# Kernel tuning notes

Measured on AMD Instinct MI355X. Metric: run time of the kernel, lower is better.

## Reference

```python
import jax, jax.numpy as jnp
import numpy as np

B, T, C, H = 4, 2048, 1024, 16
D = C // H  # head dim 64


def setup_inputs() -> dict:
    key = jax.random.key(0)
    ks = jax.random.split(key, 5)
    s = 1.0 / np.sqrt(C)
    return {
        "x": jax.random.normal(ks[0], (B, T, C), jnp.float32),
        "Wq": jax.random.normal(ks[1], (C, C), jnp.float32) * s,
        "bq": jnp.zeros((C,), jnp.float32),
        "Wk": jax.random.normal(ks[2], (C, C), jnp.float32) * s,
        "bk": jnp.zeros((C,), jnp.float32),
        "Wv": jax.random.normal(ks[3], (C, C), jnp.float32) * s,
        "bv": jnp.zeros((C,), jnp.float32),
        "Wp": jax.random.normal(ks[4], (C, C), jnp.float32) * s,
        "bp": jnp.zeros((C,), jnp.float32),
    }


def reference(x, Wq, bq, Wk, bk, Wv, bv, Wp, bp):
    # project and split heads: [B,T,C] -> [B,H,T,D]
    def heads(w, b):
        return (x @ w.T + b).reshape(B, T, H, D).transpose(0, 2, 1, 3)

    q = heads(Wq, bq)
    k = heads(Wk, bk)
    v = heads(Wv, bv)

    att = jnp.einsum("bhqd,bhkd->bhqk", q, k) * (1.0 / np.sqrt(D))
    causal = jnp.tril(jnp.ones((T, T), bool))  # [T,T]
    att = jnp.where(causal[None, None], att, -jnp.inf)
    att = jax.nn.softmax(att, axis=-1)
    # dropout prob is 0.0 -> identity
    y = jnp.einsum("bhqk,bhkd->bhqd", att, v)
    y = y.transpose(0, 2, 1, 3).reshape(B, T, C)
    return y @ Wp.T + bp
```

## Files before the change

### kernel.cpp

```cpp
#include <hip/hip_runtime.h>
#include <hip/hip_bf16.h>

#define BB 4
#define TT 2048
#define CC 1024
#define HH 16
#define DD 64
#define PSTR 72

typedef unsigned short u16;
typedef __attribute__((ext_vector_type(8))) short bf16x8;
typedef __attribute__((ext_vector_type(4))) float f32x4;
typedef __attribute__((ext_vector_type(16))) float f32x16;

__device__ __forceinline__ float bf2f(u16 v) {
    union { unsigned u; float f; } c; c.u = ((unsigned)v) << 16; return c.f;
}
__device__ __forceinline__ u16 f2bf(float f) {
    union { float f; unsigned u; } c; c.f = f;
    unsigned u = c.u + 0x7fffu + ((c.u >> 16) & 1u);
    return (u16)(u >> 16);
}
__device__ __forceinline__ float fast_exp2(float x) {
    float r;
    asm volatile("v_exp_f32 %0, %1\n\ts_nop 1" : "=v"(r) : "v"(x));
    return r;
}
__device__ __forceinline__ unsigned pack_bf16(unsigned b0, unsigned b1) {
    unsigned d;
    asm("v_perm_b32 %0, %1, %2, %3" : "=v"(d) : "v"(b1), "v"(b0), "v"(0x07060302u));
    return d;
}
__device__ __forceinline__ uint2 pack4(float v0, float v1, float v2, float v3) {
    uint2 pk;
    pk.x = pack_bf16(__float_as_uint(v0) + 0x8000u, __float_as_uint(v1) + 0x8000u);
    pk.y = pack_bf16(__float_as_uint(v2) + 0x8000u, __float_as_uint(v3) + 0x8000u);
    return pk;
}
__device__ __forceinline__ void gload16(const u16* g, u16* l) {
    __builtin_amdgcn_global_load_lds(
        (const __attribute__((address_space(1))) void*)g,
        (__attribute__((address_space(3))) void*)l, 16, 0, 0);
}

__device__ __forceinline__ int detect_bf16(const u16* __restrict__ xprobe, int* sh) {
    const int t = threadIdx.x;
    u16 hh = xprobe[2 * t];
    int e = (hh >> 7) & 0xFF;
    unsigned long long m = __ballot(e >= 118 && e <= 132);
    if ((t & 63) == 0) sh[t >> 6] = __popcll(m);
    __syncthreads();
    return (sh[0] + sh[1] + sh[2] + sh[3]) >= 128;
}

struct CastArgs {
    const void* src[9];
    u16* dst[9];
    int blk_start[10];
    int n[9];
};
__global__ __launch_bounds__(256) void cast_all(CastArgs a, const u16* __restrict__ xprobe) {
    __shared__ int sh[4];
    const int isbf = detect_bf16(xprobe, sh);
    int b = blockIdx.x;
    int s = 0;
    while (s < 8 && b >= a.blk_start[s + 1]) s++;
    int i0 = (b - a.blk_start[s]) * 2048 + threadIdx.x * 8;
    if (i0 + 8 > a.n[s]) return;
    if (isbf) {
        *(uint4*)&a.dst[s][i0] = *(const uint4*)&((const u16*)a.src[s])[i0];
    } else {
        const float* sp = (const float*)a.src[s];
        u16 tmp[8];
#pragma unroll
        for (int j = 0; j < 8; j++) tmp[j] = f2bf(sp[i0 + j]);
        *(uint4*)&a.dst[s][i0] = *(uint4*)tmp;
    }
}

__device__ __forceinline__ void gemm_core(
    const u16* __restrict__ X, const u16* __restrict__ W,
    u16* Als, u16* Bls, f32x16 (&acc)[2][2],
    int m0, int n0, int wave, int lane, int wm, int wn)
{
    const int l32 = lane & 31;
    const int hv  = lane >> 5;
    int srow[4], sch[4];
#pragma unroll
    for (int c = 0; c < 4; c++) {
        srow[c] = wave * 32 + c * 8 + (lane >> 3);
        sch[c]  = (lane & 7) ^ (srow[c] & 7);
    }

    for (int k0 = 0; k0 < CC; k0 += 64) {
        __syncthreads();
#pragma unroll
        for (int c = 0; c < 4; c++) {
            gload16(&X[(size_t)(m0 + srow[c]) * CC + k0 + sch[c] * 8],
                    &Als[wave * 2048 + c * 512]);
            gload16(&W[(size_t)(n0 + srow[c]) * CC + k0 + sch[c] * 8],
                    &Bls[wave * 2048 + c * 512]);
        }
        __syncthreads();

#pragma unroll
        for (int ks = 0; ks < 4; ks++) {
            const int sw = ((ks * 2 + hv) ^ (l32 & 7)) * 8;
            bf16x8 a[2], b[2];
#pragma unroll
            for (int i = 0; i < 2; i++)
                a[i] = *(const bf16x8*)&Als[(wm + i * 32 + l32) * 64 + sw];
#pragma unroll
            for (int j = 0; j < 2; j++)
                b[j] = *(const bf16x8*)&Bls[(wn + j * 32 + l32) * 64 + sw];
#pragma unroll
            for (int i = 0; i < 2; i++)
#pragma unroll
                for (int j = 0; j < 2; j++)
                    acc[i][j] = __builtin_amdgcn_mfma_f32_32x32x16_bf16(
                        b[j], a[i], acc[i][j], 0, 0, 0);
        }
    }
}

__global__ __launch_bounds__(256, 2) void gemm_qkv(
    const u16* __restrict__ X,
    const u16* __restrict__ Wq, const u16* __restrict__ Wk, const u16* __restrict__ Wv,
    const u16* __restrict__ bq, const u16* __restrict__ bk, const u16* __restrict__ bv,
    u16* __restrict__ Q, u16* __restrict__ K, u16* __restrict__ VT)
{
    __shared__ __align__(16) u16 Als[128 * 64];
    __shared__ __align__(16) u16 Bls[3 * 128 * 64];

    const int tid  = threadIdx.x;
    const int wave = tid >> 6;
    const int lane = tid & 63;
    const int l32  = lane & 31;
    const int hv   = lane >> 5;
    const int m0   = blockIdx.x * 128;
    const int n0   = blockIdx.y * 128;
    const int wm   = (wave >> 1) * 64;
    const int wn   = (wave & 1) * 64;

    const u16* Ws[3]  = {Wq, Wk, Wv};

    f32x16 acc[3][2][2];
#pragma unroll
    for (int z = 0; z < 3; z++)
#pragma unroll
        for (int i = 0; i < 2; i++)
#pragma unroll
            for (int j = 0; j < 2; j++) acc[z][i][j] = (f32x16)0.0f;

    int srow[4], sch[4];
#pragma unroll
    for (int c = 0; c < 4; c++) {
        srow[c] = wave * 32 + c * 8 + (lane >> 3);
        sch[c]  = (lane & 7) ^ (srow[c] & 7);
    }

    for (int k0 = 0; k0 < CC; k0 += 64) {
        __syncthreads();
#pragma unroll
        for (int c = 0; c < 4; c++)
            gload16(&X[(size_t)(m0 + srow[c]) * CC + k0 + sch[c] * 8],
                    &Als[wave * 2048 + c * 512]);
#pragma unroll
        for (int z = 0; z < 3; z++)
#pragma unroll
            for (int c = 0; c < 4; c++)
                gload16(&Ws[z][(size_t)(n0 + srow[c]) * CC + k0 + sch[c] * 8],
                        &Bls[z * 8192 + wave * 2048 + c * 512]);
        __syncthreads();

#pragma unroll
        for (int ks = 0; ks < 4; ks++) {
            const int sw = ((ks * 2 + hv) ^ (l32 & 7)) * 8;
            bf16x8 a[2];
#pragma unroll
            for (int i = 0; i < 2; i++)
                a[i] = *(const bf16x8*)&Als[(wm + i * 32 + l32) * 64 + sw];
#pragma unroll
            for (int z = 0; z < 3; z++) {
                bf16x8 b[2];
#pragma unroll
                for (int j = 0; j < 2; j++)
                    b[j] = *(const bf16x8*)&Bls[z * 8192 + (wn + j * 32 + l32) * 64 + sw];
#pragma unroll
                for (int i = 0; i < 2; i++)
#pragma unroll
                    for (int j = 0; j < 2; j++)
                        acc[z][i][j] = __builtin_amdgcn_mfma_f32_32x32x16_bf16(
                            b[j], a[i], acc[z][i][j], 0, 0, 0);
            }
        }
    }

    const u16* biases[3] = {bq, bk, bv};
    u16* outs[3]         = {Q, K, VT};

#pragma unroll
    for (int z = 0; z < 3; z++) {
        const float scale = (z == 0) ? 0.18033688f : 1.0f;
        const u16* bias = biases[z];
        u16* outp = outs[z];
#pragma unroll
        for (int j = 0; j < 2; j++) {
#pragma unroll
            for (int rq = 0; rq < 4; rq++) {
                const int n_base = n0 + wn + j * 32 + rq * 8 + hv * 4;
                union { uint2 u; u16 us[4]; } braw;
                braw.u = *(const uint2*)&bias[n_base];
                const int hh = n_base >> 6, d0 = n_base & 63;
#pragma unroll
                for (int i = 0; i < 2; i++) {
                    const int m = m0 + wm + i * 32 + l32;
                    const int bb = m >> 11, t = m & (TT - 1);
                    float v0 = (acc[z][i][j][rq * 4 + 0] + bf2f(braw.us[0])) * scale;
                    float v1 = (acc[z][i][j][rq * 4 + 1] + bf2f(braw.us[1])) * scale;
                    float v2 = (acc[z][i][j][rq * 4 + 2] + bf2f(braw.us[2])) * scale;
                    float v3 = (acc[z][i][j][rq * 4 + 3] + bf2f(braw.us[3])) * scale;
                    if (z < 2) {
                        *(uint2*)&outp[((size_t)(bb * HH + hh) * TT + t) * DD + d0] =
                            pack4(v0, v1, v2, v3);
                    } else {
                        const size_t base = (size_t)(bb * HH + hh) * DD * TT + t;
                        outp[base + (size_t)(d0 + 0) * TT] = f2bf(v0);
                        outp[base + (size_t)(d0 + 1) * TT] = f2bf(v1);
                        outp[base + (size_t)(d0 + 2) * TT] = f2bf(v2);
                        outp[base + (size_t)(d0 + 3) * TT] = f2bf(v3);
                    }
                }
            }
        }
    }
}

__global__ __launch_bounds__(256, 4) void gemm_proj(
    const u16* __restrict__ X, const u16* __restrict__ W,
    const u16* __restrict__ bias, void* __restrict__ out,
    const u16* __restrict__ xprobe)
{
    __shared__ __align__(16) u16 Als[128 * 64];
    __shared__ __align__(16) u16 Bls[128 * 64];
    __shared__ int sh[4];

    const int isbf = detect_bf16(xprobe, sh);

    const int tid  = threadIdx.x;
    const int wave = tid >> 6;
    const int lane = tid & 63;
    const int l32  = lane & 31;
    const int hv   = lane >> 5;
    const int m0   = blockIdx.x * 128;
    const int n0   = blockIdx.y * 128;
    const int wm   = (wave >> 1) * 64;
    const int wn   = (wave & 1) * 64;

    f32x16 acc[2][2];
#pragma unroll
    for (int i = 0; i < 2; i++)
#pragma unroll
        for (int j = 0; j < 2; j++) acc[i][j] = (f32x16)0.0f;

    gemm_core(X, W, Als, Bls, acc, m0, n0, wave, lane, wm, wn);

#pragma unroll
    for (int j = 0; j < 2; j++) {
#pragma unroll
        for (int rq = 0; rq < 4; rq++) {
            const int n_base = n0 + wn + j * 32 + rq * 8 + hv * 4;
            union { uint2 u; u16 us[4]; } braw;
            braw.u = *(const uint2*)&bias[n_base];
#pragma unroll
            for (int i = 0; i < 2; i++) {
                const int m = m0 + wm + i * 32 + l32;
                float v0 = acc[i][j][rq * 4 + 0] + bf2f(braw.us[0]);
                float v1 = acc[i][j][rq * 4 + 1] + bf2f(braw.us[1]);
                float v2 = acc[i][j][rq * 4 + 2] + bf2f(braw.us[2]);
                float v3 = acc[i][j][rq * 4 + 3] + bf2f(braw.us[3]);
                if (isbf) {
                    *(uint2*)&((u16*)out)[(size_t)m * CC + n_base] = pack4(v0, v1, v2, v3);
                } else {
                    float4 f; f.x = v0; f.y = v1; f.z = v2; f.w = v3;
                    *(float4*)&((float*)out)[(size_t)m * CC + n_base] = f;
                }
            }
        }
    }
}

__global__ __launch_bounds__(256, 4) void attn_kernel(
    const u16* __restrict__ Qg, const u16* __restrict__ Kg,
    const u16* __restrict__ VTg, u16* __restrict__ Yg)
{
    __shared__ __align__(16) u16 Ks[64 * 64];
    __shared__ __align__(16) u16 VTs[64 * 64];
    __shared__ __align__(16) u16 Ps[128 * PSTR];
    __shared__ float ls[128];

    const int tid  = threadIdx.x;
    const int wave = tid >> 6;
    const int lane = tid & 63;
    const int quad = lane >> 4;
    const int l16  = lane & 15;
    const int ly   = (l16 & 7) ^ (l16 >> 3);
    const int bh    = blockIdx.x;
    const int qtile = (TT / 128 - 1) - blockIdx.y;
    const int h = bh & (HH - 1);
    const int b = bh >> 4;
    const int q0 = qtile * 128;

    bf16x8 qf[2][2];
#pragma unroll
    for (int g = 0; g < 2; g++)
#pragma unroll
        for (int ks = 0; ks < 2; ks++)
            qf[g][ks] = *(const bf16x8*)&Qg[((size_t)bh * TT + q0 + wave * 32 +
                                             g * 16 + l16) * DD + ks * 32 + quad * 8];

    const u16* kp[2];
    const u16* vp[2];
#pragma unroll
    for (int c = 0; c < 2; c++) {
        const int srow = wave * 16 + c * 8 + (lane >> 3);
        const int sch  = (lane & 7) ^ (lane >> 3) ^ ((wave * 2 + c) & 7);
        kp[c] = Kg + (size_t)bh * TT * DD + (size_t)srow * DD + sch * 8;
        vp[c] = VTg + (size_t)bh * DD * TT + (size_t)srow * TT + sch * 8;
    }

    f32x4 o_acc[2][4];
#pragma unroll
    for (int g = 0; g < 2; g++)
#pragma unroll
        for (int jt = 0; jt < 4; jt++) o_acc[g][jt] = (f32x4)0.0f;
    float lsum[2] = {0.0f, 0.0f};

    const int ntiles = 2 * qtile;

    for (int kv = 0; kv < ntiles + 2; kv++) {
        const bool masked = (kv >= ntiles);
        __syncthreads();
#pragma unroll
        for (int c = 0; c < 2; c++) {
            gload16(kp[c], &Ks[wave * 1024 + c * 512]);
            gload16(vp[c], &VTs[wave * 1024 + c * 512]);
            kp[c] += 64 * DD;
            vp[c] += 64;
        }
        __syncthreads();

        f32x4 st[2][4];
#pragma unroll
        for (int g = 0; g < 2; g++)
#pragma unroll
            for (int j = 0; j < 4; j++) st[g][j] = (f32x4)0.0f;
#pragma unroll
        for (int ks = 0; ks < 2; ks++) {
            const int rsw = ((ks * 4 + quad) ^ ly) * 8;
#pragma unroll
            for (int j = 0; j < 4; j++) {
                bf16x8 kf = *(const bf16x8*)&Ks[(j * 16 + l16) * 64 + (rsw ^ (j * 16))];
#pragma unroll
                for (int g = 0; g < 2; g++)
                    st[g][j] = __builtin_amdgcn_mfma_f32_16x16x32_bf16(
                        kf, qf[g][ks], st[g][j], 0, 0, 0);
            }
        }

#pragma unroll
        for (int g = 0; g < 2; g++) {
            u16* psrow = &Ps[(wave * 32 + g * 16 + l16) * PSTR];
            const int qrow = q0 + wave * 32 + g * 16 + l16;
            float lp = 0.0f;
#pragma unroll
            for (int j = 0; j < 4; j++) {
                float e0 = fast_exp2(st[g][j][0]);
                float e1 = fast_exp2(st[g][j][1]);
                float e2 = fast_exp2(st[g][j][2]);
                float e3 = fast_exp2(st[g][j][3]);
                if (masked) {
                    const int kc = kv * 64 + j * 16 + quad * 4;
                    if (kc + 0 > qrow) e0 = 0.0f;
                    if (kc + 1 > qrow) e1 = 0.0f;
                    if (kc + 2 > qrow) e2 = 0.0f;
                    if (kc + 3 > qrow) e3 = 0.0f;
                }
                lp += (e0 + e1) + (e2 + e3);
                uint2 pk;
                pk.x = pack_bf16(__float_as_uint(e0) + 0x8000u,
                                 __float_as_uint(e1) + 0x8000u);
                pk.y = pack_bf16(__float_as_uint(e2) + 0x8000u,
                                 __float_as_uint(e3) + 0x8000u);
                *(uint2*)&psrow[j * 16 + quad * 4] = pk;
            }
            lsum[g] += lp;
        }

#pragma unroll
        for (int ks = 0; ks < 2; ks++) {
            const int rsw = ((ks * 4 + quad) ^ ly) * 8;
            bf16x8 vfk[4];
#pragma unroll
            for (int jt = 0; jt < 4; jt++)
                vfk[jt] = *(const bf16x8*)&VTs[(jt * 16 + l16) * 64 + (rsw ^ (jt * 16))];
#pragma unroll
            for (int g = 0; g < 2; g++) {
                bf16x8 pf = *(const bf16x8*)&Ps[(wave * 32 + g * 16 + l16) * PSTR +
                                                ks * 32 + quad * 8];
#pragma unroll
                for (int jt = 0; jt < 4; jt++)
                    o_acc[g][jt] = __builtin_amdgcn_mfma_f32_16x16x32_bf16(
                        pf, vfk[jt], o_acc[g][jt], 0, 0, 0);
            }
        }
    }

#pragma unroll
    for (int g = 0; g < 2; g++) {
        lsum[g] += __shfl_xor(lsum[g], 16, 64);
        lsum[g] += __shfl_xor(lsum[g], 32, 64);
        ls[wave * 32 + g * 16 + l16] = lsum[g];
    }

#pragma unroll
    for (int g = 0; g < 2; g++) {
        float linv[4];
#pragma unroll
        for (int r = 0; r < 4; r++)
            linv[r] = 1.0f / fmaxf(ls[wave * 32 + g * 16 + quad * 4 + r], 1e-20f);
#pragma unroll
        for (int jt = 0; jt < 4; jt++) {
#pragma unroll
            for (int r = 0; r < 4; r++) {
                const int t = q0 + wave * 32 + g * 16 + quad * 4 + r;
                const int c = h * DD + jt * 16 + l16;
                Yg[((size_t)b * TT + t) * CC + c] = f2bf(o_acc[g][jt][r] * linv[r]);
            }
        }
    }
}

extern "C" void kernel_launch(void* const* d_in, const int* in_sizes, int n_in,
                              void* d_out, int out_size, void* d_ws, size_t ws_size,
                              hipStream_t stream) {
    u16* w = (u16*)d_ws;
    size_t off = 0;
    const size_t NX = (size_t)BB * TT * CC;
    const size_t NW = (size_t)CC * CC;
    const size_t NB = CC;
    const size_t per = (size_t)BB * HH * TT * DD;

    u16* xb  = w + off; off += NX;
    u16* Wqb = w + off; off += NW;
    u16* Wkb = w + off; off += NW;
    u16* Wvb = w + off; off += NW;
    u16* Wpb = w + off; off += NW;
    u16* bqb = w + off; off += NB;
    u16* bkb = w + off; off += NB;
    u16* bvb = w + off; off += NB;
    u16* bpb = w + off; off += NB;
    u16* Q   = w + off; off += per;
    u16* K   = w + off; off += per;
    u16* VT  = w + off; off += per;
    u16* Y   = w + off; off += per;

    CastArgs ca;
    const int srcmap[9] = {0, 1, 3, 5, 7, 2, 4, 6, 8};
    u16* dsts[9] = {xb, Wqb, Wkb, Wvb, Wpb, bqb, bkb, bvb, bpb};
    int ns[9] = {(int)NX, (int)NW, (int)NW, (int)NW, (int)NW,
                 (int)NB, (int)NB, (int)NB, (int)NB};
    int acc_blk = 0;
    for (int i = 0; i < 9; i++) {
        ca.src[i] = d_in[srcmap[i]];
        ca.dst[i] = dsts[i];
        ca.n[i]   = ns[i];
        ca.blk_start[i] = acc_blk;
        acc_blk += (ns[i] + 2047) / 2048;
    }
    ca.blk_start[9] = acc_blk;
    cast_all<<<acc_blk, 256, 0, stream>>>(ca, (const u16*)d_in[0]);

    gemm_qkv<<<dim3(64, 8), 256, 0, stream>>>(xb, Wqb, Wkb, Wvb,
                                              bqb, bkb, bvb, Q, K, VT);
    attn_kernel<<<dim3(BB * HH, TT / 128), 256, 0, stream>>>(Q, K, VT, Y);
    gemm_proj<<<dim3(64, 8), 256, 0, stream>>>(Y, Wpb, bpb, d_out,
                                               (const u16*)d_in[0]);
}
```

Measured before the change: 256.8 us.

## Double-buffer K/V tiles in LDS and prefetch the next tile during compute

```diff
diff --git a/kernel.cpp b/kernel.cpp
--- a/kernel.cpp
+++ b/kernel.cpp
@@ -36,6 +36,11 @@
     pk.x = pack_bf16(__float_as_uint(v0) + 0x8000u, __float_as_uint(v1) + 0x8000u);
     pk.y = pack_bf16(__float_as_uint(v2) + 0x8000u, __float_as_uint(v3) + 0x8000u);
     return pk;
+}
+__device__ __forceinline__ unsigned cvtpk_bf16(float lo, float hi) {
+    unsigned r;
+    asm("v_cvt_pk_bf16_f32 %0, %1, %2" : "=v"(r) : "v"(lo), "v"(hi));
+    return r;
 }
 __device__ __forceinline__ void gload16(const u16* g, u16* l) {
     __builtin_amdgcn_global_load_lds(
@@ -290,12 +295,12 @@
     }
 }
 
-__global__ __launch_bounds__(256, 4) void attn_kernel(
+__global__ __launch_bounds__(256, 3) void attn_kernel(
     const u16* __restrict__ Qg, const u16* __restrict__ Kg,
     const u16* __restrict__ VTg, u16* __restrict__ Yg)
 {
-    __shared__ __align__(16) u16 Ks[64 * 64];
-    __shared__ __align__(16) u16 VTs[64 * 64];
+    __shared__ __align__(16) u16 Ks[2][64 * 64];
+    __shared__ __align__(16) u16 VTs[2][64 * 64];
     __shared__ __align__(16) u16 Ps[128 * PSTR];
     __shared__ float ls[128];
 
@@ -337,18 +342,29 @@
     float lsum[2] = {0.0f, 0.0f};
 
     const int ntiles = 2 * qtile;
-
-    for (int kv = 0; kv < ntiles + 2; kv++) {
+    const int nkv    = ntiles + 2;
+
+#pragma unroll
+    for (int c = 0; c < 2; c++) {
+        gload16(kp[c], &Ks[0][wave * 1024 + c * 512]);
+        gload16(vp[c], &VTs[0][wave * 1024 + c * 512]);
+        kp[c] += 64 * DD;
+        vp[c] += 64;
+    }
+
+    for (int kv = 0; kv < nkv; kv++) {
         const bool masked = (kv >= ntiles);
+        const int cur = kv & 1;
         __syncthreads();
-#pragma unroll
-        for (int c = 0; c < 2; c++) {
-            gload16(kp[c], &Ks[wave * 1024 + c * 512]);
-            gload16(vp[c], &VTs[wave * 1024 + c * 512]);
-            kp[c] += 64 * DD;
-            vp[c] += 64;
-        }
-        __syncthreads();
+        if (kv + 1 < nkv) {
+#pragma unroll
+            for (int c = 0; c < 2; c++) {
+                gload16(kp[c], &Ks[cur ^ 1][wave * 1024 + c * 512]);
+                gload16(vp[c], &VTs[cur ^ 1][wave * 1024 + c * 512]);
+                kp[c] += 64 * DD;
+                vp[c] += 64;
+            }
+        }
 
         f32x4 st[2][4];
 #pragma unroll
@@ -360,7 +376,7 @@
             const int rsw = ((ks * 4 + quad) ^ ly) * 8;
 #pragma unroll
             for (int j = 0; j < 4; j++) {
-                bf16x8 kf = *(const bf16x8*)&Ks[(j * 16 + l16) * 64 + (rsw ^ (j * 16))];
+                bf16x8 kf = *(const bf16x8*)&Ks[cur][(j * 16 + l16) * 64 + (rsw ^ (j * 16))];
 #pragma unroll
                 for (int g = 0; g < 2; g++)
                     st[g][j] = __builtin_amdgcn_mfma_f32_16x16x32_bf16(
@@ -388,10 +404,8 @@
                 }
                 lp += (e0 + e1) + (e2 + e3);
                 uint2 pk;
-                pk.x = pack_bf16(__float_as_uint(e0) + 0x8000u,
-                                 __float_as_uint(e1) + 0x8000u);
-                pk.y = pack_bf16(__float_as_uint(e2) + 0x8000u,
-                                 __float_as_uint(e3) + 0x8000u);
+                pk.x = cvtpk_bf16(e0, e1);
+                pk.y = cvtpk_bf16(e2, e3);
                 *(uint2*)&psrow[j * 16 + quad * 4] = pk;
             }
             lsum[g] += lp;
@@ -403,7 +417,7 @@
             bf16x8 vfk[4];
 #pragma unroll
             for (int jt = 0; jt < 4; jt++)
-                vfk[jt] = *(const bf16x8*)&VTs[(jt * 16 + l16) * 64 + (rsw ^ (jt * 16))];
+                vfk[jt] = *(const bf16x8*)&VTs[cur][(jt * 16 + l16) * 64 + (rsw ^ (jt * 16))];
 #pragma unroll
             for (int g = 0; g < 2; g++) {
                 bf16x8 pf = *(const bf16x8*)&Ps[(wave * 32 + g * 16 + l16) * PSTR +
```

After: 243.4 us (median of 2 runs). -5.2%, faster.
